# Kernel tuning notes

Measured on AMD Instinct MI355X. Metric: run time of the kernel, lower is better.

## Reference

```python
import jax, jax.numpy as jnp
import numpy as np

B, S, D = 16, 1024, 512
H = 2048
E = 16
TOP_K = 4


def setup_inputs() -> dict:
    key = jax.random.key(0)
    ks = jax.random.split(key, 8)
    scale = 0.02
    x = jax.random.normal(ks[0], (B, S, D), dtype=jnp.float32)
    router_w = jax.random.normal(ks[1], (D, E), dtype=jnp.float32) * scale
    router_b = jax.random.normal(ks[2], (E,), dtype=jnp.float32) * scale
    w1 = jax.random.normal(ks[3], (E, D, H), dtype=jnp.float32) * scale
    b1 = jax.random.normal(ks[4], (E, H), dtype=jnp.float32) * scale
    w2 = jax.random.normal(ks[5], (E, H, D), dtype=jnp.float32) * scale
    b2 = jax.random.normal(ks[6], (E, D), dtype=jnp.float32) * scale
    return {"x": x, "router_w": router_w, "router_b": router_b,
            "w1": w1, "b1": b1, "w2": w2, "b2": b2}


def reference(x, router_w, router_b, w1, b1, w2, b2):
    # x: [B, S, D] -> flatten tokens
    x_flat = x.reshape(-1, D)                       # [T, D]
    logits = x_flat @ router_w + router_b           # [T, E]
    top_vals, top_idx = jax.lax.top_k(logits, TOP_K)  # [T, K]
    gates = jax.nn.softmax(top_vals, axis=-1)       # softmax over selected experts only
    # Combined per-expert gate weight per token: sum over k slots routed to e.
    onehot = jax.nn.one_hot(top_idx, E, dtype=x.dtype)  # [T, K, E]
    comb = jnp.einsum('tk,tke->te', gates, onehot)      # [T, E]
    out = jnp.zeros_like(x_flat)
    for e in range(E):  # fixed small expert count
        h = jax.nn.relu(x_flat @ w1[e] + b1[e])     # [T, H]
        y = h @ w2[e] + b2[e]                       # [T, D]
        out = out + comb[:, e:e + 1] * y
    return out.reshape(x.shape)
```

## Files before the change

kernel.cpp:

```cpp
#include <hip/hip_runtime.h>
#include <stdint.h>

#define T_TOK 16384
#define DIM 512
#define HID 2048
#define NE 16
#define TOPK 4
#define BM 128
#define BN 128
#define BK 64
#define PAIR_CAP 67584
#define MAX_TILES 528
#define NB_CNT 64

typedef short s8v __attribute__((ext_vector_type(8)));
typedef float f4v __attribute__((ext_vector_type(4)));
typedef unsigned int u4v __attribute__((ext_vector_type(4)));

__device__ __forceinline__ unsigned short f2bf(float f) {
  unsigned int u = __builtin_bit_cast(unsigned int, f);
  u = (u + 0x7fffu + ((u >> 16) & 1u)) >> 16;
  return (unsigned short)u;
}
__device__ __forceinline__ float bf2f(unsigned short h) {
  return __builtin_bit_cast(float, (unsigned int)h << 16);
}

__device__ __forceinline__ void gload16(const void* g, void* l) {
  __builtin_amdgcn_global_load_lds(
      (const __attribute__((address_space(1))) unsigned int*)(uintptr_t)g,
      (__attribute__((address_space(3))) unsigned int*)(uintptr_t)l,
      16, 0, 0);
}

__global__ __launch_bounds__(256) void k_transpose_cast(const float* __restrict__ src,
                                                        unsigned short* __restrict__ dst,
                                                        int R, int C) {
  __shared__ float tile[32][33];
  size_t zo = (size_t)blockIdx.z * R * C;
  src += zo; dst += zo;
  int c0 = blockIdx.x * 32, r0 = blockIdx.y * 32;
  int tx = threadIdx.x, ty = threadIdx.y;
#pragma unroll
  for (int i = 0; i < 4; ++i)
    tile[ty + 8 * i][tx] = src[(size_t)(r0 + ty + 8 * i) * C + c0 + tx];
  __syncthreads();
#pragma unroll
  for (int i = 0; i < 4; ++i)
    dst[(size_t)(c0 + ty + 8 * i) * R + r0 + tx] = f2bf(tile[tx][ty + 8 * i]);
}

__global__ __launch_bounds__(256) void k_router(const float* __restrict__ x,
                                                const float* __restrict__ rw,
                                                const float* __restrict__ rb,
                                                int* __restrict__ topki,
                                                float* __restrict__ topkg,
                                                unsigned short* __restrict__ xb) {
  int wv = threadIdx.x >> 6, lane = threadIdx.x & 63;
  int t = blockIdx.x * 4 + wv;
  const float* xr = x + (size_t)t * DIM;
  unsigned short* xbr = xb + (size_t)t * DIM;
  double acc[NE];
#pragma unroll
  for (int e = 0; e < NE; ++e) acc[e] = 0.0;
  for (int it = 0; it < DIM / 64; ++it) {
    float xv = xr[it * 64 + lane];
    xbr[it * 64 + lane] = f2bf(xv);
    const float* r = rw + (size_t)(it * 64 + lane) * NE;
#pragma unroll
    for (int e = 0; e < NE; ++e) acc[e] += (double)xv * (double)r[e];
  }
#pragma unroll
  for (int off = 32; off >= 1; off >>= 1) {
#pragma unroll
    for (int e = 0; e < NE; ++e) acc[e] += __shfl_xor(acc[e], off, 64);
  }
  if (lane == 0) {
    float v[NE];
#pragma unroll
    for (int e = 0; e < NE; ++e) v[e] = (float)acc[e] + rb[e];
    int idx[TOPK]; float val[TOPK];
#pragma unroll
    for (int k = 0; k < TOPK; ++k) {
      float best = -1e30f; int bi = 0;
#pragma unroll
      for (int e = 0; e < NE; ++e)
        if (v[e] > best) { best = v[e]; bi = e; }
      idx[k] = bi; val[k] = best; v[bi] = -1e30f;
    }
    float m = val[0], s = 0.f, g[TOPK];
#pragma unroll
    for (int k = 0; k < TOPK; ++k) { g[k] = __expf(val[k] - m); s += g[k]; }
    float inv = 1.f / s;
#pragma unroll
    for (int k = 0; k < TOPK; ++k) {
      topki[t * TOPK + k] = idx[k];
      topkg[t * TOPK + k] = g[k] * inv;
    }
  }
}

__global__ __launch_bounds__(256) void k_count(const int* __restrict__ topki,
                                               int* __restrict__ meta) {
  __shared__ int lcnt[NE];
  int tid = threadIdx.x;
  if (tid < NE) lcnt[tid] = 0;
  __syncthreads();
  int base = blockIdx.x * 1024 + tid * 4;
#pragma unroll
  for (int j = 0; j < 4; ++j) atomicAdd(&lcnt[topki[base + j]], 1);
  __syncthreads();
  if (tid < NE) meta[1056 + blockIdx.x * NE + tid] = lcnt[tid];
}

__global__ __launch_bounds__(256) void k_plan(int* __restrict__ meta,
                                              int* __restrict__ ptok,
                                              float* __restrict__ pgate) {
  __shared__ int cnt_s[NE], po_s[NE + 1];
  int tid = threadIdx.x;
  if (tid < NE) {
    int s = 0;
    for (int b = 0; b < NB_CNT; ++b) s += meta[1056 + b * NE + tid];
    cnt_s[tid] = s;
  }
  __syncthreads();
  if (tid == 0) {
    int off = 0;
    for (int e = 0; e < NE; ++e) {
      po_s[e] = off;
      meta[1 + e] = off;
      off += ((cnt_s[e] + BM - 1) / BM) * BM;
    }
    po_s[NE] = off;
    meta[1 + NE] = off;
    meta[0] = off / BM;
  }
  __syncthreads();
  if (tid < NE) {
    int run = po_s[tid];
    for (int b = 0; b < NB_CNT; ++b) {
      meta[32 + b * NE + tid] = run;
      run += meta[1056 + b * NE + tid];
    }
  }
  for (int e = 0; e < NE; ++e) {
    int start = po_s[e] + cnt_s[e], end = po_s[e + 1];
    for (int i = start + tid; i < end; i += 256) { ptok[i] = 0; pgate[i] = 0.f; }
  }
}

__global__ __launch_bounds__(256) void k_scatter(const int* __restrict__ topki,
                                                 const float* __restrict__ topkg,
                                                 const int* __restrict__ meta,
                                                 int* __restrict__ ptok,
                                                 float* __restrict__ pgate,
                                                 int* __restrict__ sinv) {
  __shared__ int lcnt[NE];
  int tid = threadIdx.x;
  if (tid < NE) lcnt[tid] = 0;
  __syncthreads();
  int base = blockIdx.x * 1024 + tid * 4;
#pragma unroll
  for (int j = 0; j < 4; ++j) {
    int i = base + j;
    int e = topki[i];
    int r = atomicAdd(&lcnt[e], 1);
    int slot = meta[32 + blockIdx.x * NE + e] + r;
    ptok[slot] = i >> 2;
    pgate[slot] = topkg[i];
    sinv[i] = slot;
  }
}

__global__ __launch_bounds__(256) void k_pipe(const unsigned short* __restrict__ xb,
                                              const unsigned short* __restrict__ w1t,
                                              const float* __restrict__ b1,
                                              const unsigned short* __restrict__ w2t,
                                              const float* __restrict__ b2,
                                              const int* __restrict__ ptok,
                                              const float* __restrict__ pgate,
                                              const int* __restrict__ meta,
                                              unsigned short* __restrict__ hdst,
                                              const unsigned short* __restrict__ hsrc,
                                              unsigned short* __restrict__ yslot,
                                              float* __restrict__ out,
                                              int c1, int c2, int C) {
  __shared__ __align__(16) unsigned short Al[BM * BK];
  __shared__ __align__(16) unsigned short Bl[BN * BK];
  int tid = threadIdx.x;
  int lane = tid & 63, w = tid >> 6;
  int wm = w >> 1, wn = w & 1;
  int w4 = w * 4096;
  int sub = lane >> 3;
  int lg = (lane & 7) ^ sub;
  int lrow = lane & 15, quad = lane >> 4;
  int r7 = lrow & 7;

  if (blockIdx.x < 16) {
    if (c1 < 0) return;
    int tile = c1 * C + blockIdx.y;
    if (tile >= meta[0]) return;
    int row0 = tile * BM;
    int e = 0;
#pragma unroll
    for (int i = 1; i < NE; ++i)
      if (row0 >= meta[1 + i]) e = i;
    int nblock = blockIdx.x * BN;
    const unsigned short* asrc[4];
    const unsigned short* bsrc[4];
#pragma unroll
    for (int t = 0; t < 4; ++t) {
      int r = w * 32 + t * 8 + sub;
      asrc[t] = xb + (size_t)ptok[row0 + r] * DIM + lg * 8;
      bsrc[t] = w1t + ((size_t)e * HID + nblock + r) * DIM + lg * 8;
    }
    f4v acc[4][4] = {};
    for (int k0 = 0; k0 < DIM; k0 += BK) {
#pragma unroll
      for (int t = 0; t < 4; ++t) gload16(asrc[t] + k0, (char*)Al + w4 + t * 1024);
#pragma unroll
      for (int t = 0; t < 4; ++t) gload16(bsrc[t] + k0, (char*)Bl + w4 + t * 1024);
      __syncthreads();
#pragma unroll
      for (int ks = 0; ks < 2; ++ks) {
        int pg = ((ks * 4 + quad) ^ r7) * 8;
        s8v af[4], bfr[4];
#pragma unroll
        for (int mt = 0; mt < 4; ++mt)
          af[mt] = __builtin_bit_cast(s8v, *(const u4v*)&Al[(wm * 64 + mt * 16 + lrow) * BK + pg]);
#pragma unroll
        for (int nt = 0; nt < 4; ++nt)
          bfr[nt] = __builtin_bit_cast(s8v, *(const u4v*)&Bl[(wn * 64 + nt * 16 + lrow) * BK + pg]);
#pragma unroll
        for (int mt = 0; mt < 4; ++mt) {
#pragma unroll
          for (int nt = 0; nt < 4; ++nt)
            acc[mt][nt] = __builtin_amdgcn_mfma_f32_16x16x32_bf16(af[mt], bfr[nt], acc[mt][nt], 0, 0, 0);
        }
      }
      __syncthreads();
    }
    size_t hrow0 = (size_t)blockIdx.y * BM;
#pragma unroll
    for (int nt = 0; nt < 4; ++nt) {
      int gcol = nblock + wn * 64 + nt * 16 + lrow;
      float bias = b1[e * HID + gcol];
#pragma unroll
      for (int mt = 0; mt < 4; ++mt) {
#pragma unroll
        for (int j = 0; j < 4; ++j) {
          int grow = wm * 64 + mt * 16 + quad * 4 + j;
          float v = acc[mt][nt][j] + bias;
          hdst[(hrow0 + grow) * HID + gcol] = f2bf(v > 0.f ? v : 0.f);
        }
      }
    }
  } else {
    if (c2 < 0) return;
    int tile = c2 * C + blockIdx.y;
    if (tile >= meta[0]) return;
    int row0 = tile * BM;
    int e = 0;
#pragma unroll
    for (int i = 1; i < NE; ++i)
      if (row0 >= meta[1 + i]) e = i;
    int nblock = (blockIdx.x - 16) * BN;
    const unsigned short* asrc[4];
    const unsigned short* bsrc[4];
#pragma unroll
    for (int t = 0; t < 4; ++t) {
      int r = w * 32 + t * 8 + sub;
      asrc[t] = hsrc + ((size_t)blockIdx.y * BM + r) * HID + lg * 8;
      bsrc[t] = w2t + ((size_t)e * DIM + nblock + r) * HID + lg * 8;
    }
    f4v acc[4][4] = {};
    for (int k0 = 0; k0 < HID; k0 += BK) {
#pragma unroll
      for (int t = 0; t < 4; ++t) gload16(asrc[t] + k0, (char*)Al + w4 + t * 1024);
#pragma unroll
      for (int t = 0; t < 4; ++t) gload16(bsrc[t] + k0, (char*)Bl + w4 + t * 1024);
      __syncthreads();
#pragma unroll
      for (int ks = 0; ks < 2; ++ks) {
        int pg = ((ks * 4 + quad) ^ r7) * 8;
        s8v af[4], bfr[4];
#pragma unroll
        for (int mt = 0; mt < 4; ++mt)
          af[mt] = __builtin_bit_cast(s8v, *(const u4v*)&Al[(wm * 64 + mt * 16 + lrow) * BK + pg]);
#pragma unroll
        for (int nt = 0; nt < 4; ++nt)
          bfr[nt] = __builtin_bit_cast(s8v, *(const u4v*)&Bl[(wn * 64 + nt * 16 + lrow) * BK + pg]);
#pragma unroll
        for (int mt = 0; mt < 4; ++mt) {
#pragma unroll
          for (int nt = 0; nt < 4; ++nt)
            acc[mt][nt] = __builtin_amdgcn_mfma_f32_16x16x32_bf16(af[mt], bfr[nt], acc[mt][nt], 0, 0, 0);
        }
      }
      __syncthreads();
    }
    float bias[4];
#pragma unroll
    for (int nt = 0; nt < 4; ++nt)
      bias[nt] = b2[e * DIM + nblock + wn * 64 + nt * 16 + lrow];
    if (yslot) {
#pragma unroll
      for (int mt = 0; mt < 4; ++mt) {
#pragma unroll
        for (int j = 0; j < 4; ++j) {
          int p = row0 + wm * 64 + mt * 16 + quad * 4 + j;
          float g = pgate[p];
          unsigned short* yr = yslot + (size_t)p * DIM + nblock + wn * 64 + lrow;
#pragma unroll
          for (int nt = 0; nt < 4; ++nt)
            yr[nt * 16] = f2bf(g * (acc[mt][nt][j] + bias[nt]));
        }
      }
    } else {
#pragma unroll
      for (int mt = 0; mt < 4; ++mt) {
#pragma unroll
        for (int j = 0; j < 4; ++j) {
          int p = row0 + wm * 64 + mt * 16 + quad * 4 + j;
          float g = pgate[p];
          if (g != 0.f) {
            int tok = ptok[p];
            float* orow = out + (size_t)tok * DIM + nblock + wn * 64 + lrow;
#pragma unroll
            for (int nt = 0; nt < 4; ++nt)
              atomicAdd(orow + nt * 16, g * (acc[mt][nt][j] + bias[nt]));
          }
        }
      }
    }
  }
}

__global__ __launch_bounds__(256) void k_gather(const unsigned short* __restrict__ yslot,
                                                const int* __restrict__ sinv,
                                                float* __restrict__ out) {
  int id = blockIdx.x * 256 + threadIdx.x;
  int t = id >> 7, d4 = (id & 127) << 2;
  int4 s = *(const int4*)(sinv + t * 4);
  int sl[4] = {s.x, s.y, s.z, s.w};
  float sum0 = 0.f, sum1 = 0.f, sum2 = 0.f, sum3 = 0.f;
#pragma unroll
  for (int k = 0; k < 4; ++k) {
    ushort4 v = *(const ushort4*)(yslot + (size_t)sl[k] * DIM + d4);
    sum0 += bf2f(v.x); sum1 += bf2f(v.y); sum2 += bf2f(v.z); sum3 += bf2f(v.w);
  }
  float4 r; r.x = sum0; r.y = sum1; r.z = sum2; r.w = sum3;
  *(float4*)(out + (size_t)t * DIM + d4) = r;
}

extern "C" void kernel_launch(void* const* d_in, const int* in_sizes, int n_in,
                              void* d_out, int out_size, void* d_ws, size_t ws_size,
                              hipStream_t stream) {
  const float* x  = (const float*)d_in[0];
  const float* rw = (const float*)d_in[1];
  const float* rb = (const float*)d_in[2];
  const float* w1 = (const float*)d_in[3];
  const float* b1 = (const float*)d_in[4];
  const float* w2 = (const float*)d_in[5];
  const float* b2 = (const float*)d_in[6];
  float* out = (float*)d_out;
  char* ws = (char*)d_ws;

  size_t o_xb    = 0;
  size_t o_w1t   = o_xb    + (size_t)T_TOK * DIM * 2;
  size_t o_w2t   = o_w1t   + (size_t)NE * DIM * HID * 2;
  size_t o_topki = o_w2t   + (size_t)NE * DIM * HID * 2;
  size_t o_topkg = o_topki + (size_t)T_TOK * TOPK * 4;
  size_t o_meta  = o_topkg + (size_t)T_TOK * TOPK * 4;
  size_t o_ptok  = o_meta  + 16384;
  size_t o_pgate = o_ptok  + (size_t)PAIR_CAP * 4;
  size_t o_sinv  = o_pgate + (size_t)PAIR_CAP * 4;
  size_t o_yslot = o_sinv  + (size_t)T_TOK * TOPK * 4;
  size_t o_hb    = o_yslot + (size_t)PAIR_CAP * DIM * 2;

  unsigned short* xb   = (unsigned short*)(ws + o_xb);
  unsigned short* w1t  = (unsigned short*)(ws + o_w1t);
  unsigned short* w2t  = (unsigned short*)(ws + o_w2t);
  int*            tki  = (int*)(ws + o_topki);
  float*          tkg  = (float*)(ws + o_topkg);
  int*            meta = (int*)(ws + o_meta);
  int*            ptok = (int*)(ws + o_ptok);
  float*          pgt  = (float*)(ws + o_pgate);
  int*            sinv = (int*)(ws + o_sinv);

  size_t tile_h = (size_t)BM * HID * 2;
  size_t avail = ws_size > o_hb ? ws_size - o_hb : 0;
  long Cd = (long)(avail / (2 * tile_h));
  int use_slot = Cd >= 1;

  k_router<<<T_TOK / 4, 256, 0, stream>>>(x, rw, rb, tki, tkg, xb);
  k_transpose_cast<<<dim3(HID / 32, DIM / 32, NE), dim3(32, 8), 0, stream>>>(w1, w1t, DIM, HID);
  k_transpose_cast<<<dim3(DIM / 32, HID / 32, NE), dim3(32, 8), 0, stream>>>(w2, w2t, HID, DIM);
  k_count<<<NB_CNT, 256, 0, stream>>>(tki, meta);
  k_plan<<<1, 256, 0, stream>>>(meta, ptok, pgt);
  k_scatter<<<NB_CNT, 256, 0, stream>>>(tki, tkg, meta, ptok, pgt, sinv);

  if (use_slot) {
    unsigned short* ysl = (unsigned short*)(ws + o_yslot);
    int C = (int)(Cd > MAX_TILES ? MAX_TILES : Cd);
    int n_chunks = (MAX_TILES + C - 1) / C;
    unsigned short* hb0 = (unsigned short*)(ws + o_hb);
    unsigned short* hb1 = hb0 + (size_t)C * BM * HID;
    for (int i = 0; i <= n_chunks; ++i) {
      unsigned short* dst = (i & 1) ? hb1 : hb0;
      unsigned short* src = (i & 1) ? hb0 : hb1;
      int c1 = (i < n_chunks) ? i : -1;
      int c2 = i - 1;
      k_pipe<<<dim3(20, C), 256, 0, stream>>>(xb, w1t, b1, w2t, b2, ptok, pgt, meta,
                                              dst, src, ysl, out, c1, c2, C);
    }
    k_gather<<<T_TOK * DIM / 4 / 256, 256, 0, stream>>>(ysl, sinv, out);
  } else {
    long Cf = (long)((ws_size - o_yslot) / tile_h);
    int C = (int)(Cf < 1 ? 1 : (Cf > MAX_TILES ? MAX_TILES : Cf));
    int n_chunks = (MAX_TILES + C - 1) / C;
    unsigned short* hb = (unsigned short*)(ws + o_yslot);
    hipMemsetAsync(d_out, 0, (size_t)T_TOK * DIM * 4, stream);
    for (int i = 0; i < n_chunks; ++i) {
      k_pipe<<<dim3(20, C), 256, 0, stream>>>(xb, w1t, b1, w2t, b2, ptok, pgt, meta,
                                              hb, hb, nullptr, out, i, -1, C);
      k_pipe<<<dim3(20, C), 256, 0, stream>>>(xb, w1t, b1, w2t, b2, ptok, pgt, meta,
                                              hb, hb, nullptr, out, -1, i, C);
    }
  }
}
```

Measured before the change: 727.9 us.

## Use 256x256 tiles with 8 waves and double-buffered, phased LDS pipeline in expert GEMMs

Grows the grouped GEMM tile from 128x128 to 256x256 with 512 threads per block. It double-buffers LDS and splits each K step into quadrant phases that interleave staged global-to-LDS loads with MFMA work, using explicit waitcnt, barriers and setprio. The aim is more data reuse per loaded byte and hiding of global load latency behind compute. In exchange, larger tiles mean more padding waste per expert (PAIR_CAP grows) and fewer blocks. It also brings higher register pressure and more fragile hand-written synchronisation.

```diff
diff --git a/kernel.cpp b/kernel.cpp
--- a/kernel.cpp
+++ b/kernel.cpp
@@ -6,11 +6,11 @@
 #define HID 2048
 #define NE 16
 #define TOPK 4
-#define BM 128
-#define BN 128
-#define BK 64
-#define PAIR_CAP 67584
-#define MAX_TILES 528
+#define BM 256
+#define BN 256
+#define BKT 64
+#define PAIR_CAP 69632
+#define MAX_TILES 272
 #define NB_CNT 64
 
 typedef short s8v __attribute__((ext_vector_type(8)));
@@ -172,163 +172,229 @@
   }
 }
 
-__global__ __launch_bounds__(256) void k_pipe(const unsigned short* __restrict__ xb,
-                                              const unsigned short* __restrict__ w1t,
-                                              const float* __restrict__ b1,
-                                              const unsigned short* __restrict__ w2t,
-                                              const float* __restrict__ b2,
-                                              const int* __restrict__ ptok,
-                                              const float* __restrict__ pgate,
-                                              const int* __restrict__ meta,
-                                              unsigned short* __restrict__ hdst,
-                                              const unsigned short* __restrict__ hsrc,
-                                              unsigned short* __restrict__ yslot,
-                                              float* __restrict__ out,
-                                              int c1, int c2, int C) {
-  __shared__ __align__(16) unsigned short Al[BM * BK];
-  __shared__ __align__(16) unsigned short Bl[BN * BK];
+
+#define MBAR() asm volatile("s_barrier" ::: "memory")
+#define EBAR() asm volatile("s_barrier" ::: "memory")
+#define SP1() __builtin_amdgcn_s_setprio(1)
+#define SP0() __builtin_amdgcn_s_setprio(0)
+#define LGK0() do { asm volatile("s_waitcnt lgkmcnt(0)" ::: "memory"); \
+                    __builtin_amdgcn_sched_barrier(0); } while (0)
+#define VMC(n) asm volatile("s_waitcnt vmcnt(" #n ")" ::: "memory")
+#define NOP ((void)0)
+
+#define STG(rg, kt, c) do {                                                            \
+    int _k = (kt) * BKT;                                                               \
+    if ((rg) < 2) {                                                                    \
+      gload16(aP[rg][0] + _k, (char*)&Al[c][0] + (rg) * 16384 + w * 1024);             \
+      gload16(aP[rg][1] + _k, (char*)&Al[c][0] + (rg) * 16384 + 8192 + w * 1024);      \
+    } else {                                                                           \
+      gload16(bP[(rg) - 2][0] + _k, (char*)&Bl[c][0] + ((rg) - 2) * 16384 + w * 1024); \
+      gload16(bP[(rg) - 2][1] + _k, (char*)&Bl[c][0] + ((rg) - 2) * 16384 + 8192 + w * 1024); \
+    }                                                                                  \
+  } while (0)
+
+#define RDA(c, mq) do {                                                                \
+    _Pragma("unroll")                                                                  \
+    for (int mt = 0; mt < 4; ++mt) {                                                   \
+      af[mt][0] = __builtin_bit_cast(s8v, *(const u4v*)&Al[c][(mq) * 8192 + aoff + mt * 1024 + cs0]); \
+      af[mt][1] = __builtin_bit_cast(s8v, *(const u4v*)&Al[c][(mq) * 8192 + aoff + mt * 1024 + cs1]); \
+    }                                                                                  \
+  } while (0)
+
+#define RDB(c, nq) do {                                                                \
+    _Pragma("unroll")                                                                  \
+    for (int nt = 0; nt < 2; ++nt) {                                                   \
+      bfr[nt][0] = __builtin_bit_cast(s8v, *(const u4v*)&Bl[c][(nq) * 8192 + boff + nt * 1024 + cs0]); \
+      bfr[nt][1] = __builtin_bit_cast(s8v, *(const u4v*)&Bl[c][(nq) * 8192 + boff + nt * 1024 + cs1]); \
+    }                                                                                  \
+  } while (0)
+
+#define MMQ(mq, nq) do {                                                               \
+    _Pragma("unroll")                                                                  \
+    for (int mt = 0; mt < 4; ++mt) {                                                   \
+      _Pragma("unroll")                                                                \
+      for (int nt = 0; nt < 2; ++nt) {                                                 \
+        acc[(mq) * 4 + mt][(nq) * 2 + nt] = __builtin_amdgcn_mfma_f32_16x16x32_bf16(   \
+            af[mt][0], bfr[nt][0], acc[(mq) * 4 + mt][(nq) * 2 + nt], 0, 0, 0);        \
+        acc[(mq) * 4 + mt][(nq) * 2 + nt] = __builtin_amdgcn_mfma_f32_16x16x32_bf16(   \
+            af[mt][1], bfr[nt][1], acc[(mq) * 4 + mt][(nq) * 2 + nt], 0, 0, 0);        \
+      }                                                                                \
+    }                                                                                  \
+  } while (0)
+
+#define PH(c, mq, nq, doA, STAGE, WAITC) do {  \
+    if (doA) RDA(c, mq);                       \
+    RDB(c, nq);                                \
+    STAGE;                                     \
+    MBAR();                                    \
+    LGK0();                                    \
+    SP1(); MMQ(mq, nq); SP0();                 \
+    WAITC;                                     \
+    EBAR();                                    \
+  } while (0)
+
+__global__ __launch_bounds__(512, 2) void k_pipe(const unsigned short* __restrict__ xb,
+                                                 const unsigned short* __restrict__ w1t,
+                                                 const float* __restrict__ b1,
+                                                 const unsigned short* __restrict__ w2t,
+                                                 const float* __restrict__ b2,
+                                                 const int* __restrict__ ptok,
+                                                 const float* __restrict__ pgate,
+                                                 const int* __restrict__ meta,
+                                                 unsigned short* __restrict__ hdst,
+                                                 const unsigned short* __restrict__ hsrc,
+                                                 unsigned short* __restrict__ yslot,
+                                                 float* __restrict__ out,
+                                                 int c1, int c2, int C) {
+  __shared__ __align__(16) unsigned short Al[2][BM * BKT];
+  __shared__ __align__(16) unsigned short Bl[2][BN * BKT];
   int tid = threadIdx.x;
   int lane = tid & 63, w = tid >> 6;
-  int wm = w >> 1, wn = w & 1;
-  int w4 = w * 4096;
-  int sub = lane >> 3;
-  int lg = (lane & 7) ^ sub;
+  int wm = w >> 2, wn = w & 3;
   int lrow = lane & 15, quad = lane >> 4;
   int r7 = lrow & 7;
-
-  if (blockIdx.x < 16) {
-    if (c1 < 0) return;
-    int tile = c1 * C + blockIdx.y;
-    if (tile >= meta[0]) return;
-    int row0 = tile * BM;
-    int e = 0;
-#pragma unroll
-    for (int i = 1; i < NE; ++i)
-      if (row0 >= meta[1 + i]) e = i;
-    int nblock = blockIdx.x * BN;
-    const unsigned short* asrc[4];
-    const unsigned short* bsrc[4];
-#pragma unroll
-    for (int t = 0; t < 4; ++t) {
-      int r = w * 32 + t * 8 + sub;
-      asrc[t] = xb + (size_t)ptok[row0 + r] * DIM + lg * 8;
-      bsrc[t] = w1t + ((size_t)e * HID + nblock + r) * DIM + lg * 8;
-    }
-    f4v acc[4][4] = {};
-    for (int k0 = 0; k0 < DIM; k0 += BK) {
-#pragma unroll
-      for (int t = 0; t < 4; ++t) gload16(asrc[t] + k0, (char*)Al + w4 + t * 1024);
-#pragma unroll
-      for (int t = 0; t < 4; ++t) gload16(bsrc[t] + k0, (char*)Bl + w4 + t * 1024);
-      __syncthreads();
-#pragma unroll
-      for (int ks = 0; ks < 2; ++ks) {
-        int pg = ((ks * 4 + quad) ^ r7) * 8;
-        s8v af[4], bfr[4];
-#pragma unroll
-        for (int mt = 0; mt < 4; ++mt)
-          af[mt] = __builtin_bit_cast(s8v, *(const u4v*)&Al[(wm * 64 + mt * 16 + lrow) * BK + pg]);
-#pragma unroll
-        for (int nt = 0; nt < 4; ++nt)
-          bfr[nt] = __builtin_bit_cast(s8v, *(const u4v*)&Bl[(wn * 64 + nt * 16 + lrow) * BK + pg]);
-#pragma unroll
-        for (int mt = 0; mt < 4; ++mt) {
-#pragma unroll
-          for (int nt = 0; nt < 4; ++nt)
-            acc[mt][nt] = __builtin_amdgcn_mfma_f32_16x16x32_bf16(af[mt], bfr[nt], acc[mt][nt], 0, 0, 0);
+  int sub = lane >> 3, lg = (lane & 7) ^ sub;
+
+  bool g2 = blockIdx.x < 2;
+  int chunk = g2 ? c2 : c1;
+  if (chunk < 0) return;
+  int tile = chunk * C + blockIdx.y;
+  if (tile >= meta[0]) return;
+  int row0 = tile * BM;
+  int e = 0;
+#pragma unroll
+  for (int i = 1; i < NE; ++i)
+    if (row0 >= meta[1 + i]) e = i;
+  int nblock = g2 ? (int)blockIdx.x * BN : ((int)blockIdx.x - 2) * BN;
+
+  const unsigned short* aP[2][2];
+  const unsigned short* bP[2][2];
+  int NKT;
+  if (!g2) {
+    NKT = DIM / BKT;
+#pragma unroll
+    for (int h = 0; h < 2; ++h)
+#pragma unroll
+      for (int t = 0; t < 2; ++t) {
+        int r = h * 128 + t * 64 + w * 8 + sub;
+        aP[h][t] = xb + (size_t)ptok[row0 + r] * DIM + lg * 8;
+        bP[h][t] = w1t + ((size_t)e * HID + nblock + r) * DIM + lg * 8;
+      }
+  } else {
+    NKT = HID / BKT;
+#pragma unroll
+    for (int h = 0; h < 2; ++h)
+#pragma unroll
+      for (int t = 0; t < 2; ++t) {
+        int r = h * 128 + t * 64 + w * 8 + sub;
+        aP[h][t] = hsrc + ((size_t)blockIdx.y * BM + r) * HID + lg * 8;
+        bP[h][t] = w2t + ((size_t)e * DIM + nblock + r) * HID + lg * 8;
+      }
+  }
+
+  int aoff = (wm * 64 + lrow) * BKT;
+  int boff = (wn * 32 + lrow) * BKT;
+  int cs0 = (quad ^ r7) * 8;
+  int cs1 = ((4 + quad) ^ r7) * 8;
+
+  f4v acc[8][4] = {};
+  s8v af[4][2];
+  s8v bfr[2][2];
+
+  STG(0, 0, 0); STG(2, 0, 0); STG(1, 0, 0); STG(3, 0, 0);
+  STG(0, 1, 1); STG(2, 1, 1);
+  VMC(8);
+  EBAR();
+
+  int NI = NKT >> 1;
+  for (int i = 0; i < NI - 1; ++i) {
+    int bt = 2 * i;
+    PH(0, 0, 0, true,  STG(1, bt + 1, 1), VMC(6));
+    PH(0, 0, 1, false, STG(3, bt + 1, 1), NOP);
+    PH(0, 1, 0, true,  STG(0, bt + 2, 0), NOP);
+    PH(0, 1, 1, false, STG(2, bt + 2, 0), VMC(8));
+    PH(1, 0, 0, true,  STG(1, bt + 2, 0), VMC(6));
+    PH(1, 0, 1, false, STG(3, bt + 2, 0), NOP);
+    PH(1, 1, 0, true,  STG(0, bt + 3, 1), NOP);
+    PH(1, 1, 1, false, STG(2, bt + 3, 1), VMC(8));
+  }
+  {
+    int bt = NKT - 2;
+    PH(0, 0, 0, true,  STG(1, bt + 1, 1), VMC(6));
+    PH(0, 0, 1, false, STG(3, bt + 1, 1), NOP);
+    PH(0, 1, 0, true,  NOP, NOP);
+    PH(0, 1, 1, false, NOP, VMC(4));
+    PH(1, 0, 0, true,  NOP, VMC(0));
+    PH(1, 0, 1, false, NOP, NOP);
+    PH(1, 1, 0, true,  NOP, NOP);
+    PH(1, 1, 1, false, NOP, NOP);
+  }
+
+  if (!g2) {
+    size_t hrow0 = (size_t)blockIdx.y * BM;
+#pragma unroll
+    for (int nq = 0; nq < 2; ++nq) {
+#pragma unroll
+      for (int nt = 0; nt < 2; ++nt) {
+        int gcol = nblock + nq * 128 + wn * 32 + nt * 16 + lrow;
+        float bias = b1[e * HID + gcol];
+#pragma unroll
+        for (int mq = 0; mq < 2; ++mq) {
+#pragma unroll
+          for (int mt = 0; mt < 4; ++mt) {
+#pragma unroll
+            for (int j = 0; j < 4; ++j) {
+              int grow = mq * 128 + wm * 64 + mt * 16 + quad * 4 + j;
+              float v = acc[mq * 4 + mt][nq * 2 + nt][j] + bias;
+              hdst[(hrow0 + grow) * HID + gcol] = f2bf(v > 0.f ? v : 0.f);
+            }
+          }
         }
       }
-      __syncthreads();
-    }
-    size_t hrow0 = (size_t)blockIdx.y * BM;
-#pragma unroll
-    for (int nt = 0; nt < 4; ++nt) {
-      int gcol = nblock + wn * 64 + nt * 16 + lrow;
-      float bias = b1[e * HID + gcol];
-#pragma unroll
-      for (int mt = 0; mt < 4; ++mt) {
-#pragma unroll
-        for (int j = 0; j < 4; ++j) {
-          int grow = wm * 64 + mt * 16 + quad * 4 + j;
-          float v = acc[mt][nt][j] + bias;
-          hdst[(hrow0 + grow) * HID + gcol] = f2bf(v > 0.f ? v : 0.f);
-        }
-      }
     }
   } else {
-    if (c2 < 0) return;
-    int tile = c2 * C + blockIdx.y;
-    if (tile >= meta[0]) return;
-    int row0 = tile * BM;
-    int e = 0;
-#pragma unroll
-    for (int i = 1; i < NE; ++i)
-      if (row0 >= meta[1 + i]) e = i;
-    int nblock = (blockIdx.x - 16) * BN;
-    const unsigned short* asrc[4];
-    const unsigned short* bsrc[4];
-#pragma unroll
-    for (int t = 0; t < 4; ++t) {
-      int r = w * 32 + t * 8 + sub;
-      asrc[t] = hsrc + ((size_t)blockIdx.y * BM + r) * HID + lg * 8;
-      bsrc[t] = w2t + ((size_t)e * DIM + nblock + r) * HID + lg * 8;
-    }
-    f4v acc[4][4] = {};
-    for (int k0 = 0; k0 < HID; k0 += BK) {
-#pragma unroll
-      for (int t = 0; t < 4; ++t) gload16(asrc[t] + k0, (char*)Al + w4 + t * 1024);
-#pragma unroll
-      for (int t = 0; t < 4; ++t) gload16(bsrc[t] + k0, (char*)Bl + w4 + t * 1024);
-      __syncthreads();
-#pragma unroll
-      for (int ks = 0; ks < 2; ++ks) {
-        int pg = ((ks * 4 + quad) ^ r7) * 8;
-        s8v af[4], bfr[4];
-#pragma unroll
-        for (int mt = 0; mt < 4; ++mt)
-          af[mt] = __builtin_bit_cast(s8v, *(const u4v*)&Al[(wm * 64 + mt * 16 + lrow) * BK + pg]);
-#pragma unroll
-        for (int nt = 0; nt < 4; ++nt)
-          bfr[nt] = __builtin_bit_cast(s8v, *(const u4v*)&Bl[(wn * 64 + nt * 16 + lrow) * BK + pg]);
+    float bias[2][2];
+#pragma unroll
+    for (int nq = 0; nq < 2; ++nq)
+#pragma unroll
+      for (int nt = 0; nt < 2; ++nt)
+        bias[nq][nt] = b2[e * DIM + nblock + nq * 128 + wn * 32 + nt * 16 + lrow];
+    if (yslot) {
+#pragma unroll
+      for (int mq = 0; mq < 2; ++mq) {
 #pragma unroll
         for (int mt = 0; mt < 4; ++mt) {
 #pragma unroll
-          for (int nt = 0; nt < 4; ++nt)
-            acc[mt][nt] = __builtin_amdgcn_mfma_f32_16x16x32_bf16(af[mt], bfr[nt], acc[mt][nt], 0, 0, 0);
-        }
-      }
-      __syncthreads();
-    }
-    float bias[4];
-#pragma unroll
-    for (int nt = 0; nt < 4; ++nt)
-      bias[nt] = b2[e * DIM + nblock + wn * 64 + nt * 16 + lrow];
-    if (yslot) {
-#pragma unroll
-      for (int mt = 0; mt < 4; ++mt) {
-#pragma unroll
-        for (int j = 0; j < 4; ++j) {
-          int p = row0 + wm * 64 + mt * 16 + quad * 4 + j;
-          float g = pgate[p];
-          unsigned short* yr = yslot + (size_t)p * DIM + nblock + wn * 64 + lrow;
-#pragma unroll
-          for (int nt = 0; nt < 4; ++nt)
-            yr[nt * 16] = f2bf(g * (acc[mt][nt][j] + bias[nt]));
+          for (int j = 0; j < 4; ++j) {
+            int p = row0 + mq * 128 + wm * 64 + mt * 16 + quad * 4 + j;
+            float g = pgate[p];
+            unsigned short* yr = yslot + (size_t)p * DIM + nblock + wn * 32 + lrow;
+#pragma unroll
+            for (int nq = 0; nq < 2; ++nq)
+#pragma unroll
+              for (int nt = 0; nt < 2; ++nt)
+                yr[nq * 128 + nt * 16] = f2bf(g * (acc[mq * 4 + mt][nq * 2 + nt][j] + bias[nq][nt]));
+          }
         }
       }
     } else {
 #pragma unroll
-      for (int mt = 0; mt < 4; ++mt) {
-#pragma unroll
-        for (int j = 0; j < 4; ++j) {
-          int p = row0 + wm * 64 + mt * 16 + quad * 4 + j;
-          float g = pgate[p];
-          if (g != 0.f) {
-            int tok = ptok[p];
-            float* orow = out + (size_t)tok * DIM + nblock + wn * 64 + lrow;
-#pragma unroll
-            for (int nt = 0; nt < 4; ++nt)
-              atomicAdd(orow + nt * 16, g * (acc[mt][nt][j] + bias[nt]));
+      for (int mq = 0; mq < 2; ++mq) {
+#pragma unroll
+        for (int mt = 0; mt < 4; ++mt) {
+#pragma unroll
+          for (int j = 0; j < 4; ++j) {
+            int p = row0 + mq * 128 + wm * 64 + mt * 16 + quad * 4 + j;
+            float g = pgate[p];
+            if (g != 0.f) {
+              int tok = ptok[p];
+              float* orow = out + (size_t)tok * DIM + nblock + wn * 32 + lrow;
+#pragma unroll
+              for (int nq = 0; nq < 2; ++nq)
+#pragma unroll
+                for (int nt = 0; nt < 2; ++nt)
+                  atomicAdd(orow + nq * 128 + nt * 16, g * (acc[mq * 4 + mt][nq * 2 + nt][j] + bias[nq][nt]));
+            }
           }
         }
       }
@@ -411,7 +477,7 @@
       unsigned short* src = (i & 1) ? hb0 : hb1;
       int c1 = (i < n_chunks) ? i : -1;
       int c2 = i - 1;
-      k_pipe<<<dim3(20, C), 256, 0, stream>>>(xb, w1t, b1, w2t, b2, ptok, pgt, meta,
+      k_pipe<<<dim3(10, C), 512, 0, stream>>>(xb, w1t, b1, w2t, b2, ptok, pgt, meta,
                                               dst, src, ysl, out, c1, c2, C);
     }
     k_gather<<<T_TOK * DIM / 4 / 256, 256, 0, stream>>>(ysl, sinv, out);
@@ -422,9 +488,9 @@
     unsigned short* hb = (unsigned short*)(ws + o_yslot);
     hipMemsetAsync(d_out, 0, (size_t)T_TOK * DIM * 4, stream);
     for (int i = 0; i < n_chunks; ++i) {
-      k_pipe<<<dim3(20, C), 256, 0, stream>>>(xb, w1t, b1, w2t, b2, ptok, pgt, meta,
+      k_pipe<<<dim3(10, C), 512, 0, stream>>>(xb, w1t, b1, w2t, b2, ptok, pgt, meta,
                                               hb, hb, nullptr, out, i, -1, C);
-      k_pipe<<<dim3(20, C), 256, 0, stream>>>(xb, w1t, b1, w2t, b2, ptok, pgt, meta,
+      k_pipe<<<dim3(10, C), 512, 0, stream>>>(xb, w1t, b1, w2t, b2, ptok, pgt, meta,
                                               hb, hb, nullptr, out, -1, i, C);
     }
   }
```

New measurement: 747.6 us. +2.7%, slower.
